# Kernel tuning notes

Measured on AMD Instinct MI355X. Metric: run time of the kernel, lower is better.

Reference implementation:

```python
import jax, jax.numpy as jnp
import numpy as np

B, C, H, W = 8, 384, 32, 32
KEYS, HEADS, U = 16, 4, 1
VS = C // HEADS
N = H * W
BN_EPS = 1e-5


def setup_inputs() -> dict:
    key = jax.random.key(0)
    ks = jax.random.split(key, 8)
    x = jax.random.normal(ks[0], (B, C, H, W), dtype=jnp.float32)
    # 1x1 convs (spectral-normalized in torch; SN only rescales the weight,
    # so a plain weight matrix computes the same functional form)
    Wq = jax.random.normal(ks[1], (KEYS * HEADS, C), dtype=jnp.float32) * 0.02
    Wk = jax.random.normal(ks[2], (KEYS * U, C), dtype=jnp.float32) * 0.02
    Wv = jax.random.normal(ks[3], (VS * U, C), dtype=jnp.float32) * 0.02
    # BatchNorm affine params (torch code xavier-inits weight, zeros bias)
    gamma_q = jax.random.normal(ks[4], (KEYS * HEADS,), dtype=jnp.float32)
    beta_q = jnp.zeros((KEYS * HEADS,), dtype=jnp.float32)
    gamma_v = jax.random.normal(ks[5], (VS * U,), dtype=jnp.float32)
    beta_v = jnp.zeros((VS * U,), dtype=jnp.float32)
    pos_emb = jax.random.normal(ks[6], (N, N, KEYS, U), dtype=jnp.float32)
    return {"x": x, "Wq": Wq, "Wk": Wk, "Wv": Wv,
            "gamma_q": gamma_q, "beta_q": beta_q,
            "gamma_v": gamma_v, "beta_v": beta_v,
            "pos_emb": pos_emb}


def _bn(z, gamma, beta):
    # z: (B, Ch, N); BatchNorm2d in training mode: biased batch stats over (B, N)
    mean = jnp.mean(z, axis=(0, 2), keepdims=True)
    var = jnp.var(z, axis=(0, 2), keepdims=True)
    zn = (z - mean) * jax.lax.rsqrt(var + BN_EPS)
    return zn * gamma[None, :, None] + beta[None, :, None]


def reference(x, Wq, Wk, Wv, gamma_q, beta_q, gamma_v, beta_v, pos_emb):
    xf = x.reshape(B, C, N)                       # 1x1 conv == per-pixel matmul
    q = jnp.einsum('oc,bcn->bon', Wq, xf)         # (B, KEYS*HEADS, N)
    k = jnp.einsum('oc,bcn->bon', Wk, xf)         # (B, KEYS*U, N)
    v = jnp.einsum('oc,bcn->bon', Wv, xf)         # (B, VS*U, N)
    q = _bn(q, gamma_q, beta_q)
    v = _bn(v, gamma_v, beta_v)
    q = q.reshape(B, HEADS, KEYS, N)
    k = k.reshape(B, U, KEYS, N)
    v = v.reshape(B, U, VS, N)
    k = jax.nn.softmax(k, axis=-1)
    lambdac = jnp.einsum('bukm,buvm->bkv', k, v)          # content lambda
    Yc = jnp.einsum('bhkn,bkv->bhvn', q, lambdac)
    lambdap = jnp.einsum('nmku,buvm->bnkv', pos_emb, v)   # position lambda (B,N,K,V)
    Yp = jnp.einsum('bhkn,bnkv->bhvn', q, lambdap)
    Y = (Yc + Yp).reshape(B, C, H, W)
    return Y
```

## Files before the change

kernel.cpp:

```cpp
#include <hip/hip_runtime.h>

typedef __attribute__((ext_vector_type(8))) short short8;
typedef __attribute__((ext_vector_type(16))) float floatx16;
typedef __attribute__((ext_vector_type(4))) float floatx4;
typedef unsigned short ushort16_t;
typedef unsigned int uint32;

#define BB 8
#define CC 384
#define NPIX 1024
#define TOTCH 176
#define BN_EPS 1e-5f

__device__ __forceinline__ ushort16_t f2bf(float x) {
    uint32 u = __float_as_uint(x);
    u += 0x7FFFu + ((u >> 16) & 1u);
    return (ushort16_t)(u >> 16);
}
__device__ __forceinline__ uint32 pk2(float a, float b) {
    uint32 ua = __float_as_uint(a); ua += 0x7FFFu + ((ua >> 16) & 1u);
    uint32 ub = __float_as_uint(b); ub += 0x7FFFu + ((ub >> 16) & 1u);
    return (ua >> 16) | (ub & 0xFFFF0000u);
}
__device__ __forceinline__ int div48(int x) {
    return (int)(((unsigned)x * 21846u) >> 20);
}
#define LGKM0_ONLY 0xC07F


__global__ __launch_bounds__(256) void k_wt(const float* __restrict__ Wq,
    const float* __restrict__ Wk, const float* __restrict__ Wv,
    ushort16_t* __restrict__ wbf)
{
    int bx = blockIdx.x, t = threadIdx.x;
    #pragma unroll
    for (int jj = 0; jj < 9; ++jj) {
        int idx8 = (bx * 9 + jj) * 256 + t;
        int row = div48(idx8);
        int g   = idx8 - row * 48;
        float4 f0, f1;
        if (row < 176) {
            const float* src;
            if (row < 64)       src = Wq + (size_t)row * CC;
            else if (row < 80)  src = Wk + (size_t)(row - 64) * CC;
            else                src = Wv + (size_t)(row - 80) * CC;
            f0 = *(const float4*)(src + g * 8);
            f1 = *(const float4*)(src + g * 8 + 4);
        } else {
            f0.x = f0.y = f0.z = f0.w = 0.f;
            f1 = f0;
        }
        uint4 w;
        w.x = pk2(f0.x, f0.y); w.y = pk2(f0.z, f0.w);
        w.z = pk2(f1.x, f1.y); w.w = pk2(f1.z, f1.w);
        *(uint4*)&wbf[(size_t)row * CC + g * 8] = w;
    }
}

__global__ __launch_bounds__(256) void k_proj(const float* __restrict__ x,
    const ushort16_t* __restrict__ wbf, float* __restrict__ qkv)
{
    __shared__ __align__(16) ushort16_t XT[32 * 392];
    int bx = blockIdx.x, t = threadIdx.x;
    int b = bx >> 5, nbase = (bx & 31) * 32;
    const float* xb = x + (size_t)b * (CC * NPIX) + nbase;
    #pragma unroll
    for (int j = 0; j < 12; ++j) {
        int idx = t + 256 * j;
        int c = idx >> 3, ng = idx & 7;
        float4 f = *(const float4*)(xb + (size_t)c * NPIX + ng * 4);
        int col = ng * 4;
        XT[(col + 0) * 392 + c] = f2bf(f.x);
        XT[(col + 1) * 392 + c] = f2bf(f.y);
        XT[(col + 2) * 392 + c] = f2bf(f.z);
        XT[(col + 3) * 392 + c] = f2bf(f.w);
    }
    __syncthreads();

    int wave = t >> 6, lane = t & 63;
    int ct = wave & 1;
    int rs = wave >> 1;
    int col1 = lane & 15, kq = lane >> 4;
    const ushort16_t* bbase = &XT[(ct * 16 + col1) * 392 + kq * 8];
    int n = nbase + ct * 16 + col1;

    for (int r = rs; r < 11; r += 2) {
        int r0 = r * 16;
        const ushort16_t* ap = wbf + (size_t)(r0 + col1) * CC + kq * 8;
        floatx4 acc = {0.f, 0.f, 0.f, 0.f};
        short8 a0 = *(const short8*)ap;
        short8 b0 = *(const short8*)bbase;
        #pragma unroll
        for (int k = 1; k < 12; ++k) {
            short8 a1 = *(const short8*)(ap + k * 32);
            short8 b1 = *(const short8*)(bbase + k * 32);
            acc = __builtin_amdgcn_mfma_f32_16x16x32_bf16(a0, b0, acc, 0, 0, 0);
            a0 = a1; b0 = b1;
        }
        acc = __builtin_amdgcn_mfma_f32_16x16x32_bf16(a0, b0, acc, 0, 0, 0);
        #pragma unroll
        for (int rr = 0; rr < 4; ++rr) {
            int ch = r0 + kq * 4 + rr;
            qkv[((size_t)b * TOTCH + ch) * NPIX + n] = acc[rr];
        }
    }
}

__global__ __launch_bounds__(256) void k_bnsm(const float* __restrict__ qkv,
    const float* __restrict__ gq, const float* __restrict__ bq,
    const float* __restrict__ gv, const float* __restrict__ bv,
    float* __restrict__ sA, float* __restrict__ sB, float* __restrict__ ksm)
{
    int bx = blockIdx.x, tid = threadIdx.x;
    int wid = tid >> 6, lane = tid & 63;
    if (bx < 160) {
        int ch = bx;
        int row; float gamma, beta;
        if (ch < 64) { row = ch; gamma = gq[ch]; beta = bq[ch]; }
        else { int j = ch - 64; row = 80 + j; gamma = gv[j]; beta = bv[j]; }
        float s = 0.f, ss = 0.f;
        #pragma unroll
        for (int j = 0; j < 8; ++j) {
            int i4 = tid + 256 * j;
            int b = i4 >> 8, n4 = i4 & 255;
            float4 f = *(const float4*)(qkv + ((size_t)b * TOTCH + row) * NPIX
                                            + n4 * 4);
            s  += f.x + f.y + f.z + f.w;
            ss += f.x * f.x + f.y * f.y + f.z * f.z + f.w * f.w;
        }
        #pragma unroll
        for (int off = 32; off > 0; off >>= 1) {
            s  += __shfl_down(s, off);
            ss += __shfl_down(ss, off);
        }
        __shared__ float rs[4], rss[4];
        if (lane == 0) { rs[wid] = s; rss[wid] = ss; }
        __syncthreads();
        if (tid == 0) {
            float S  = rs[0] + rs[1] + rs[2] + rs[3];
            float SS = rss[0] + rss[1] + rss[2] + rss[3];
            float inv = 1.f / (BB * NPIX);
            float mean = S * inv;
            float var  = SS * inv - mean * mean;
            float a = gamma * rsqrtf(var + BN_EPS);
            sA[row] = a;
            sB[row] = beta - mean * a;
        }
    } else {
        int idx = bx - 160;
        int kc = idx & 15, b = idx >> 4;
        const float* rowp = qkv + ((size_t)b * TOTCH + 64 + kc) * NPIX;
        float4 v4 = *(const float4*)(rowp + tid * 4);
        float v[4] = {v4.x, v4.y, v4.z, v4.w};
        float mx = fmaxf(fmaxf(v[0], v[1]), fmaxf(v[2], v[3]));
        #pragma unroll
        for (int off = 32; off > 0; off >>= 1) mx = fmaxf(mx, __shfl_down(mx, off));
        __shared__ float sm[4], ssum[4];
        if (lane == 0) sm[wid] = mx;
        __syncthreads();
        mx = fmaxf(fmaxf(sm[0], sm[1]), fmaxf(sm[2], sm[3]));
        float e[4], s = 0.f;
        #pragma unroll
        for (int j = 0; j < 4; ++j) { e[j] = __expf(v[j] - mx); s += e[j]; }
        #pragma unroll
        for (int off = 32; off > 0; off >>= 1) s += __shfl_down(s, off);
        if (lane == 0) ssum[wid] = s;
        __syncthreads();
        float inv = 1.f / (ssum[0] + ssum[1] + ssum[2] + ssum[3]);
        float4 o;
        o.x = e[0] * inv; o.y = e[1] * inv; o.z = e[2] * inv; o.w = e[3] * inv;
        *(float4*)(ksm + ((size_t)b * 16 + kc) * NPIX + tid * 4) = o;
    }
}

__global__ __launch_bounds__(256) void k_packlc(const float* __restrict__ qkv,
    const float* __restrict__ sA, const float* __restrict__ sB,
    const float* __restrict__ ksm,
    ushort16_t* __restrict__ qt_g, ushort16_t* __restrict__ vt_g,
    ushort16_t* __restrict__ lc_g)
{
    int bx = blockIdx.x, t = threadIdx.x;
    if (bx < 128) {
        int bh = t & 31, nn = (t >> 5) & 7;
        int n = bx * 8 + nn;
        int b = bh >> 2, h = bh & 3;
        float vals[16];
        #pragma unroll
        for (int k = 0; k < 16; ++k) {
            int ch = h * 16 + k;
            vals[k] = qkv[((size_t)b * TOTCH + ch) * NPIX + n] * sA[ch] + sB[ch];
        }
        uint4 w0, w1;
        w0.x = pk2(vals[0], vals[1]);  w0.y = pk2(vals[2], vals[3]);
        w0.z = pk2(vals[4], vals[5]);  w0.w = pk2(vals[6], vals[7]);
        w1.x = pk2(vals[8], vals[9]);  w1.y = pk2(vals[10], vals[11]);
        w1.z = pk2(vals[12], vals[13]); w1.w = pk2(vals[14], vals[15]);
        *(uint4*)&qt_g[(size_t)n * 512 + bh * 8]       = w0;
        *(uint4*)&qt_g[(size_t)n * 512 + 256 + bh * 8] = w1;
    } else if (bx < 512) {
        int gi = (bx - 128) * 256 + t;
        int m8 = gi & 127;
        int vg = (gi >> 7) % 96;
        int b  = gi / (96 * 128);
        int m  = m8 * 8;
        int row = 80 + vg;
        float a = sA[row], bb = sB[row];
        const float* p = qkv + ((size_t)b * TOTCH + row) * NPIX + m;
        float4 f0 = *(const float4*)p;
        float4 f1 = *(const float4*)(p + 4);
        uint4 w;
        w.x = pk2(f0.x * a + bb, f0.y * a + bb);
        w.y = pk2(f0.z * a + bb, f0.w * a + bb);
        w.z = pk2(f1.x * a + bb, f1.y * a + bb);
        w.w = pk2(f1.z * a + bb, f1.w * a + bb);
        int mt = m >> 5, mq = (m >> 3) & 3;
        int vhh = vg / 48, vtt = (vg % 48) >> 4, vl = vg & 15;
        size_t idx = ((((size_t)b * 32 + mt) * 2 + vhh) * 3 + vtt) * 512
                   + mq * 128 + vl * 8;
        *(uint4*)&vt_g[idx] = w;
    } else {
        int gi = bx - 512;
        int v = gi % 96, b = gi / 96;
        int row = 80 + v;
        float a = sA[row], bb = sB[row];
        const float* vp = qkv + ((size_t)b * TOTCH + row) * NPIX;
        const float* kp = ksm + (size_t)b * 16 * NPIX;
        float4 vv = *(const float4*)(vp + t * 4);
        float4 vhat;
        vhat.x = vv.x * a + bb; vhat.y = vv.y * a + bb;
        vhat.z = vv.z * a + bb; vhat.w = vv.w * a + bb;
        float acc[16];
        #pragma unroll
        for (int k = 0; k < 16; ++k) {
            float4 kk = *(const float4*)(kp + (size_t)k * NPIX + t * 4);
            acc[k] = kk.x * vhat.x + kk.y * vhat.y
                   + kk.z * vhat.z + kk.w * vhat.w;
        }
        #pragma unroll
        for (int k = 0; k < 16; ++k) {
            #pragma unroll
            for (int off = 32; off > 0; off >>= 1)
                acc[k] += __shfl_down(acc[k], off);
        }
        __shared__ float red[16][4];
        int wid = t >> 6, lane = t & 63;
        if (lane == 0) {
            #pragma unroll
            for (int k = 0; k < 16; ++k) red[k][wid] = acc[k];
        }
        __syncthreads();
        int vhh = v / 48, vtt = (v % 48) >> 4, vl = v & 15;
        size_t plane = ((size_t)(b * 2 + vhh) * 3 + vtt) * 512;
        if (t < 16) {
            int k = t;
            float val = red[k][0] + red[k][1] + red[k][2] + red[k][3];
            lc_g[plane + (k >> 3) * 128 + vl * 8 + (k & 7)] = f2bf(val);
        } else if (t < 18) {
            int mq = 2 + (t - 16);
            uint4 z; z.x = z.y = z.z = z.w = 0u;
            *(uint4*)&lc_g[plane + mq * 128 + vl * 8] = z;
        }
    }
}

__global__ __launch_bounds__(512, 2) void k_main(const float* __restrict__ pos,
    const ushort16_t* __restrict__ qt_g, const ushort16_t* __restrict__ vt_g,
    const ushort16_t* __restrict__ lc_g, float* __restrict__ out)
{
    __shared__ __align__(16) ushort16_t S_s[2][8192];
    int tid  = threadIdx.x;
    int lane = tid & 63;
    int wave = tid >> 6;
    int n0 = blockIdx.x * 8;
    int vh = blockIdx.y;

    int col1 = lane & 31, half = lane >> 5;
    int pb = col1 >> 2, ph = col1 & 3;
    int pplane = pb * 2 + (ph >> 1);
    int pf = pplane & 7;
    int pcb = ph & 1;
    int b2 = wave;

    short8 qfr = *(const short8*)(qt_g + (size_t)(n0 + wave) * 512
                                  + half * 256 + col1 * 8);

    floatx4 acc[2][3];
    #pragma unroll
    for (int hg = 0; hg < 2; ++hg)
        #pragma unroll
        for (int vt = 0; vt < 3; ++vt)
            acc[hg][vt] = floatx4{0.f, 0.f, 0.f, 0.f};

    floatx16 z16;
    #pragma unroll
    for (int i = 0; i < 16; ++i) z16[i] = 0.f;

    const float* pA = pos + ((size_t)(n0 + wave) * 1024 + col1) * 16 + half * 8;
    const ushort16_t* pV = vt_g + (size_t)b2 * 98304 + (size_t)vh * 1536
                         + lane * 8;

    float4 a0c = *(const float4*)(pA);
    float4 a1c = *(const float4*)(pA + 4);
    float4 a0n = *(const float4*)(pA + 512);
    float4 a1n = *(const float4*)(pA + 516);
    short8 av0 = *(const short8*)(pV);
    short8 av1 = *(const short8*)(pV + 512);
    short8 av2 = *(const short8*)(pV + 1024);

    for (int i = 0; i < 32; ++i) {
        float4 a0nn, a1nn;
        if (i < 30) {
            const float* p = pA + (size_t)(i + 2) * 512;
            a0nn = *(const float4*)p;
            a1nn = *(const float4*)(p + 4);
        }
        short8 nv0, nv1, nv2;
        if (i < 31) {
            const ushort16_t* vp = pV + (size_t)(i + 1) * 3072;
            nv0 = *(const short8*)(vp);
            nv1 = *(const short8*)(vp + 512);
            nv2 = *(const short8*)(vp + 1024);
        }
        {
            uint4 aw;
            aw.x = pk2(a0c.x, a0c.y); aw.y = pk2(a0c.z, a0c.w);
            aw.z = pk2(a1c.x, a1c.y); aw.w = pk2(a1c.z, a1c.w);
            short8 afr = *(short8*)&aw;
            floatx16 d = __builtin_amdgcn_mfma_f32_32x32x16_bf16(
                afr, qfr, z16, 0, 0, 0);
            int nx = wave ^ pf;
            ushort16_t* Sb = S_s[i & 1];
            #pragma unroll
            for (int q = 0; q < 4; ++q) {
                int c = q * 16 + pcb * 8 + nx;
                uint2 wv;
                wv.x = pk2(d[q * 4 + 0], d[q * 4 + 1]);
                wv.y = pk2(d[q * 4 + 2], d[q * 4 + 3]);
                *(uint2*)&Sb[pplane * 512 + c * 8 + half * 4] = wv;
            }
        }
        __builtin_amdgcn_s_waitcnt(LGKM0_ONLY);
        __builtin_amdgcn_s_barrier();
        {
            const ushort16_t* Sb = S_s[i & 1];
            #pragma unroll
            for (int hg = 0; hg < 2; ++hg) {
                int p2 = b2 * 2 + hg, f2 = p2 & 7;
                short8 bs = *(const short8*)&Sb[p2 * 512
                    + ((lane >> 4) * 16 + ((lane & 15) ^ f2)) * 8];
                acc[hg][0] = __builtin_amdgcn_mfma_f32_16x16x32_bf16(
                    av0, bs, acc[hg][0], 0, 0, 0);
                acc[hg][1] = __builtin_amdgcn_mfma_f32_16x16x32_bf16(
                    av1, bs, acc[hg][1], 0, 0, 0);
                acc[hg][2] = __builtin_amdgcn_mfma_f32_16x16x32_bf16(
                    av2, bs, acc[hg][2], 0, 0, 0);
            }
        }
        a0c = a0n; a1c = a1n;
        if (i < 30) { a0n = a0nn; a1n = a1nn; }
        if (i < 31) { av0 = nv0; av1 = nv1; av2 = nv2; }
    }

    {
        const ushort16_t* lsrc = lc_g + (size_t)(b2 * 2 + vh) * 1536 + lane * 8;
        short8 lv0 = *(const short8*)(lsrc);
        short8 lv1 = *(const short8*)(lsrc + 512);
        short8 lv2 = *(const short8*)(lsrc + 1024);
        __syncthreads();
        {
            int c = half * 16 + pcb * 8 + (wave ^ pf);
            *(short8*)&S_s[0][pplane * 512 + c * 8] = qfr;
            int zp = tid >> 5, zr = tid & 31;
            int zc = (2 + (zr >> 4)) * 16 + ((zr & 15) ^ (zp & 7));
            uint4 z; z.x = z.y = z.z = z.w = 0u;
            *(uint4*)&S_s[0][zp * 512 + zc * 8] = z;
        }
        __syncthreads();
        #pragma unroll
        for (int hg = 0; hg < 2; ++hg) {
            int p2 = b2 * 2 + hg, f2 = p2 & 7;
            short8 bs = *(const short8*)&S_s[0][p2 * 512
                + ((lane >> 4) * 16 + ((lane & 15) ^ f2)) * 8];
            acc[hg][0] = __builtin_amdgcn_mfma_f32_16x16x32_bf16(
                lv0, bs, acc[hg][0], 0, 0, 0);
            acc[hg][1] = __builtin_amdgcn_mfma_f32_16x16x32_bf16(
                lv1, bs, acc[hg][1], 0, 0, 0);
            acc[hg][2] = __builtin_amdgcn_mfma_f32_16x16x32_bf16(
                lv2, bs, acc[hg][2], 0, 0, 0);
        }
    }

    {
        int cn = lane & 15;
        int nloc = cn & 7;
        #pragma unroll
        for (int hg = 0; hg < 2; ++hg) {
            int h = hg * 2 + (cn >> 3);
            #pragma unroll
            for (int vt = 0; vt < 3; ++vt) {
                #pragma unroll
                for (int r = 0; r < 4; ++r) {
                    int v = vh * 48 + vt * 16 + (lane >> 4) * 4 + r;
                    out[(size_t)(b2 * 384 + h * 96 + v) * 1024 + n0 + nloc]
                        = acc[hg][vt][r];
                }
            }
        }
    }
}

extern "C" void kernel_launch(void* const* d_in, const int* in_sizes, int n_in,
                              void* d_out, int out_size, void* d_ws, size_t ws_size,
                              hipStream_t stream) {
    const float* x   = (const float*)d_in[0];
    const float* Wq  = (const float*)d_in[1];
    const float* Wk  = (const float*)d_in[2];
    const float* Wv  = (const float*)d_in[3];
    const float* gq  = (const float*)d_in[4];
    const float* bq  = (const float*)d_in[5];
    const float* gv  = (const float*)d_in[6];
    const float* bv  = (const float*)d_in[7];
    const float* pos = (const float*)d_in[8];
    float* out = (float*)d_out;
    float* ws  = (float*)d_ws;

    float* qkv = ws;
    float* sA  = ws + 1441792;
    float* sB  = ws + 1441968;
    float* ksm = ws + 1442144;
    ushort16_t* qt_g = (ushort16_t*)(ws + 1573216);
    ushort16_t* vt_g = (ushort16_t*)(ws + 1835360);
    ushort16_t* lc_g = (ushort16_t*)(ws + 2228576);
    ushort16_t* wbf  = (ushort16_t*)(ws + 3813728);

    k_wt<<<dim3(4), dim3(256), 0, stream>>>(Wq, Wk, Wv, wbf);
    k_proj<<<dim3(256), dim3(256), 0, stream>>>(x, wbf, qkv);
    k_bnsm<<<dim3(288), dim3(256), 0, stream>>>(qkv, gq, bq, gv, bv, sA, sB, ksm);
    k_packlc<<<dim3(1280), dim3(256), 0, stream>>>(qkv, sA, sB, ksm,
                                                   qt_g, vt_g, lc_g);
    k_main<<<dim3(128, 2), dim3(512), 0, stream>>>(pos, qt_g, vt_g, lc_g, out);
}
```

Measured before the change: 172.2 us.

## Fuse BN statistics into projection and key softmax into content-lambda kernel

Removes the separate BN-stats/softmax kernel. Per-channel sums and sums of squares are now accumulated in the projection epilogue, using shuffles, shared atomics and then global atomics into a buffer that the weight-conversion kernel zeroes. The pack kernel derives the BN scale and shift per block from those sums. The content-lambda path computes the key softmax inline as an unnormalised exp-weighted sum divided by the exp sum. This saves a launch and a pass over qkv, but adds atomics and redundant per-block BN and softmax-max recomputation.

```diff
diff --git a/kernel.cpp b/kernel.cpp
--- a/kernel.cpp
+++ b/kernel.cpp
@@ -28,11 +28,14 @@
 #define LGKM0_ONLY 0xC07F
 
 
-__global__ __launch_bounds__(256) void k_wt(const float* __restrict__ Wq,
+__global__ __launch_bounds__(256, 2) void k_wt(const float* __restrict__ Wq,
     const float* __restrict__ Wk, const float* __restrict__ Wv,
-    ushort16_t* __restrict__ wbf)
+    ushort16_t* __restrict__ wbf, float* __restrict__ gsum)
 {
     int bx = blockIdx.x, t = threadIdx.x;
+    if (bx == 0) {
+        if (t < 176) { gsum[t] = 0.f; gsum[176 + t] = 0.f; }
+    }
     #pragma unroll
     for (int jj = 0; jj < 9; ++jj) {
         int idx8 = (bx * 9 + jj) * 256 + t;
@@ -57,12 +60,15 @@
     }
 }
 
-__global__ __launch_bounds__(256) void k_proj(const float* __restrict__ x,
-    const ushort16_t* __restrict__ wbf, float* __restrict__ qkv)
+__global__ __launch_bounds__(256, 2) void k_proj(const float* __restrict__ x,
+    const ushort16_t* __restrict__ wbf, float* __restrict__ qkv,
+    float* __restrict__ gsum)
 {
     __shared__ __align__(16) ushort16_t XT[32 * 392];
+    __shared__ float bsum[176], bss[176];
     int bx = blockIdx.x, t = threadIdx.x;
     int b = bx >> 5, nbase = (bx & 31) * 32;
+    if (t < 176) { bsum[t] = 0.f; bss[t] = 0.f; }
     const float* xb = x + (size_t)b * (CC * NPIX) + nbase;
     #pragma unroll
     for (int j = 0; j < 12; ++j) {
@@ -103,83 +109,51 @@
             int ch = r0 + kq * 4 + rr;
             qkv[((size_t)b * TOTCH + ch) * NPIX + n] = acc[rr];
         }
-    }
-}
-
-__global__ __launch_bounds__(256) void k_bnsm(const float* __restrict__ qkv,
+        #pragma unroll
+        for (int rr = 0; rr < 4; ++rr) {
+            float sv = acc[rr], qv = acc[rr] * acc[rr];
+            #pragma unroll
+            for (int off = 1; off < 16; off <<= 1) {
+                sv += __shfl_xor(sv, off);
+                qv += __shfl_xor(qv, off);
+            }
+            if ((lane & 15) == 0) {
+                int ch = r0 + kq * 4 + rr;
+                atomicAdd(&bsum[ch], sv);
+                atomicAdd(&bss[ch], qv);
+            }
+        }
+    }
+    __syncthreads();
+    for (int i = t; i < 176; i += 256) {
+        unsafeAtomicAdd(&gsum[i], bsum[i]);
+        unsafeAtomicAdd(&gsum[176 + i], bss[i]);
+    }
+}
+
+__global__ __launch_bounds__(256, 2) void k_packlc(const float* __restrict__ qkv,
+    const float* __restrict__ gsum,
     const float* __restrict__ gq, const float* __restrict__ bq,
     const float* __restrict__ gv, const float* __restrict__ bv,
-    float* __restrict__ sA, float* __restrict__ sB, float* __restrict__ ksm)
-{
-    int bx = blockIdx.x, tid = threadIdx.x;
-    int wid = tid >> 6, lane = tid & 63;
-    if (bx < 160) {
-        int ch = bx;
-        int row; float gamma, beta;
-        if (ch < 64) { row = ch; gamma = gq[ch]; beta = bq[ch]; }
-        else { int j = ch - 64; row = 80 + j; gamma = gv[j]; beta = bv[j]; }
-        float s = 0.f, ss = 0.f;
-        #pragma unroll
-        for (int j = 0; j < 8; ++j) {
-            int i4 = tid + 256 * j;
-            int b = i4 >> 8, n4 = i4 & 255;
-            float4 f = *(const float4*)(qkv + ((size_t)b * TOTCH + row) * NPIX
-                                            + n4 * 4);
-            s  += f.x + f.y + f.z + f.w;
-            ss += f.x * f.x + f.y * f.y + f.z * f.z + f.w * f.w;
-        }
-        #pragma unroll
-        for (int off = 32; off > 0; off >>= 1) {
-            s  += __shfl_down(s, off);
-            ss += __shfl_down(ss, off);
-        }
-        __shared__ float rs[4], rss[4];
-        if (lane == 0) { rs[wid] = s; rss[wid] = ss; }
-        __syncthreads();
-        if (tid == 0) {
-            float S  = rs[0] + rs[1] + rs[2] + rs[3];
-            float SS = rss[0] + rss[1] + rss[2] + rss[3];
-            float inv = 1.f / (BB * NPIX);
-            float mean = S * inv;
-            float var  = SS * inv - mean * mean;
-            float a = gamma * rsqrtf(var + BN_EPS);
-            sA[row] = a;
-            sB[row] = beta - mean * a;
-        }
-    } else {
-        int idx = bx - 160;
-        int kc = idx & 15, b = idx >> 4;
-        const float* rowp = qkv + ((size_t)b * TOTCH + 64 + kc) * NPIX;
-        float4 v4 = *(const float4*)(rowp + tid * 4);
-        float v[4] = {v4.x, v4.y, v4.z, v4.w};
-        float mx = fmaxf(fmaxf(v[0], v[1]), fmaxf(v[2], v[3]));
-        #pragma unroll
-        for (int off = 32; off > 0; off >>= 1) mx = fmaxf(mx, __shfl_down(mx, off));
-        __shared__ float sm[4], ssum[4];
-        if (lane == 0) sm[wid] = mx;
-        __syncthreads();
-        mx = fmaxf(fmaxf(sm[0], sm[1]), fmaxf(sm[2], sm[3]));
-        float e[4], s = 0.f;
-        #pragma unroll
-        for (int j = 0; j < 4; ++j) { e[j] = __expf(v[j] - mx); s += e[j]; }
-        #pragma unroll
-        for (int off = 32; off > 0; off >>= 1) s += __shfl_down(s, off);
-        if (lane == 0) ssum[wid] = s;
-        __syncthreads();
-        float inv = 1.f / (ssum[0] + ssum[1] + ssum[2] + ssum[3]);
-        float4 o;
-        o.x = e[0] * inv; o.y = e[1] * inv; o.z = e[2] * inv; o.w = e[3] * inv;
-        *(float4*)(ksm + ((size_t)b * 16 + kc) * NPIX + tid * 4) = o;
-    }
-}
-
-__global__ __launch_bounds__(256) void k_packlc(const float* __restrict__ qkv,
-    const float* __restrict__ sA, const float* __restrict__ sB,
-    const float* __restrict__ ksm,
     ushort16_t* __restrict__ qt_g, ushort16_t* __restrict__ vt_g,
     ushort16_t* __restrict__ lc_g)
 {
+    __shared__ float sAl[176], sBl[176];
     int bx = blockIdx.x, t = threadIdx.x;
+    if (t < 176) {
+        float g = 0.f, be = 0.f;
+        if (t < 64)       { g = gq[t];      be = bq[t]; }
+        else if (t >= 80) { g = gv[t - 80]; be = bv[t - 80]; }
+        float S = gsum[t], SS = gsum[176 + t];
+        float inv = 1.f / (BB * NPIX);
+        float mean = S * inv;
+        float var  = SS * inv - mean * mean;
+        float a = g * rsqrtf(var + BN_EPS);
+        sAl[t] = a;
+        sBl[t] = be - mean * a;
+    }
+    __syncthreads();
+
     if (bx < 128) {
         int bh = t & 31, nn = (t >> 5) & 7;
         int n = bx * 8 + nn;
@@ -188,7 +162,7 @@
         #pragma unroll
         for (int k = 0; k < 16; ++k) {
             int ch = h * 16 + k;
-            vals[k] = qkv[((size_t)b * TOTCH + ch) * NPIX + n] * sA[ch] + sB[ch];
+            vals[k] = qkv[((size_t)b * TOTCH + ch) * NPIX + n] * sAl[ch] + sBl[ch];
         }
         uint4 w0, w1;
         w0.x = pk2(vals[0], vals[1]);  w0.y = pk2(vals[2], vals[3]);
@@ -204,7 +178,7 @@
         int b  = gi / (96 * 128);
         int m  = m8 * 8;
         int row = 80 + vg;
-        float a = sA[row], bb = sB[row];
+        float a = sAl[row], bb = sBl[row];
         const float* p = qkv + ((size_t)b * TOTCH + row) * NPIX + m;
         float4 f0 = *(const float4*)p;
         float4 f1 = *(const float4*)(p + 4);
@@ -222,39 +196,66 @@
         int gi = bx - 512;
         int v = gi % 96, b = gi / 96;
         int row = 80 + v;
-        float a = sA[row], bb = sB[row];
+        float a = sAl[row], bb2 = sBl[row];
         const float* vp = qkv + ((size_t)b * TOTCH + row) * NPIX;
-        const float* kp = ksm + (size_t)b * 16 * NPIX;
+        const float* kp = qkv + ((size_t)b * TOTCH + 64) * NPIX;
         float4 vv = *(const float4*)(vp + t * 4);
         float4 vhat;
-        vhat.x = vv.x * a + bb; vhat.y = vv.y * a + bb;
-        vhat.z = vv.z * a + bb; vhat.w = vv.w * a + bb;
-        float acc[16];
+        vhat.x = vv.x * a + bb2; vhat.y = vv.y * a + bb2;
+        vhat.z = vv.z * a + bb2; vhat.w = vv.w * a + bb2;
+        int wid = t >> 6, lane = t & 63;
+
+        float4 kr[16];
+        float mx[16];
         #pragma unroll
         for (int k = 0; k < 16; ++k) {
-            float4 kk = *(const float4*)(kp + (size_t)k * NPIX + t * 4);
-            acc[k] = kk.x * vhat.x + kk.y * vhat.y
-                   + kk.z * vhat.z + kk.w * vhat.w;
-        }
+            kr[k] = *(const float4*)(kp + (size_t)k * NPIX + t * 4);
+            mx[k] = fmaxf(fmaxf(kr[k].x, kr[k].y), fmaxf(kr[k].z, kr[k].w));
+            #pragma unroll
+            for (int off = 32; off > 0; off >>= 1)
+                mx[k] = fmaxf(mx[k], __shfl_xor(mx[k], off));
+        }
+        __shared__ float xr[16][4];
+        if (lane == 0) {
+            #pragma unroll
+            for (int k = 0; k < 16; ++k) xr[k][wid] = mx[k];
+        }
+        __syncthreads();
+        #pragma unroll
+        for (int k = 0; k < 16; ++k)
+            mx[k] = fmaxf(fmaxf(xr[k][0], xr[k][1]), fmaxf(xr[k][2], xr[k][3]));
+
+        float acc[16], ps[16];
         #pragma unroll
         for (int k = 0; k < 16; ++k) {
-            #pragma unroll
-            for (int off = 32; off > 0; off >>= 1)
+            float ex = __expf(kr[k].x - mx[k]);
+            float ey = __expf(kr[k].y - mx[k]);
+            float ez = __expf(kr[k].z - mx[k]);
+            float ew = __expf(kr[k].w - mx[k]);
+            ps[k]  = ex + ey + ez + ew;
+            acc[k] = ex * vhat.x + ey * vhat.y + ez * vhat.z + ew * vhat.w;
+        }
+        #pragma unroll
+        for (int k = 0; k < 16; ++k) {
+            #pragma unroll
+            for (int off = 32; off > 0; off >>= 1) {
                 acc[k] += __shfl_down(acc[k], off);
-        }
-        __shared__ float red[16][4];
-        int wid = t >> 6, lane = t & 63;
+                ps[k]  += __shfl_down(ps[k], off);
+            }
+        }
+        __shared__ float red[16][4], red2[16][4];
         if (lane == 0) {
             #pragma unroll
-            for (int k = 0; k < 16; ++k) red[k][wid] = acc[k];
+            for (int k = 0; k < 16; ++k) { red[k][wid] = acc[k]; red2[k][wid] = ps[k]; }
         }
         __syncthreads();
         int vhh = v / 48, vtt = (v % 48) >> 4, vl = v & 15;
         size_t plane = ((size_t)(b * 2 + vhh) * 3 + vtt) * 512;
         if (t < 16) {
             int k = t;
-            float val = red[k][0] + red[k][1] + red[k][2] + red[k][3];
-            lc_g[plane + (k >> 3) * 128 + vl * 8 + (k & 7)] = f2bf(val);
+            float num = red[k][0] + red[k][1] + red[k][2] + red[k][3];
+            float den = red2[k][0] + red2[k][1] + red2[k][2] + red2[k][3];
+            lc_g[plane + (k >> 3) * 128 + vl * 8 + (k & 7)] = f2bf(num / den);
         } else if (t < 18) {
             int mq = 2 + (t - 16);
             uint4 z; z.x = z.y = z.z = z.w = 0u;
@@ -424,19 +425,16 @@
     float* out = (float*)d_out;
     float* ws  = (float*)d_ws;
 
-    float* qkv = ws;
-    float* sA  = ws + 1441792;
-    float* sB  = ws + 1441968;
-    float* ksm = ws + 1442144;
+    float* qkv  = ws;
+    float* gsum = ws + 1442144;
     ushort16_t* qt_g = (ushort16_t*)(ws + 1573216);
     ushort16_t* vt_g = (ushort16_t*)(ws + 1835360);
     ushort16_t* lc_g = (ushort16_t*)(ws + 2228576);
     ushort16_t* wbf  = (ushort16_t*)(ws + 3813728);
 
-    k_wt<<<dim3(4), dim3(256), 0, stream>>>(Wq, Wk, Wv, wbf);
-    k_proj<<<dim3(256), dim3(256), 0, stream>>>(x, wbf, qkv);
-    k_bnsm<<<dim3(288), dim3(256), 0, stream>>>(qkv, gq, bq, gv, bv, sA, sB, ksm);
-    k_packlc<<<dim3(1280), dim3(256), 0, stream>>>(qkv, sA, sB, ksm,
+    k_wt<<<dim3(4), dim3(256), 0, stream>>>(Wq, Wk, Wv, wbf, gsum);
+    k_proj<<<dim3(256), dim3(256), 0, stream>>>(x, wbf, qkv, gsum);
+    k_packlc<<<dim3(1280), dim3(256), 0, stream>>>(qkv, gsum, gq, bq, gv, bv,
                                                    qt_g, vt_g, lc_g);
     k_main<<<dim3(128, 2), dim3(512), 0, stream>>>(pos, qt_g, vt_g, lc_g, out);
 }
```

After: 185.0 us. 1.07x slower.
